# Optimization experiments

Hardware: AMD Instinct MI355X
Metric: run time of the kernel (lower is better)

Reference implementation:

```python
import jax, jax.numpy as jnp
import numpy as np


def setup_inputs() -> dict:
    key = jax.random.key(0)
    k1, k2, k3 = jax.random.split(key, 3)
    N, T, C, H, W, D = 2, 8, 3, 128, 128, 64
    images = jax.random.normal(k1, (N, T, C, H, W), dtype=jnp.float32)
    # well-conditioned pinhole intrinsics: f ~ 100, principal point near center
    K = jnp.array([[100.0, 0.0, W / 2.0], [0.0, 100.0, H / 2.0], [0.0, 0.0, 1.0]], jnp.float32)
    intrinsics = K[None, None] + 0.1 * jax.random.normal(k2, (N, T, 3, 3), dtype=jnp.float32)
    # near-identity extrinsics with small perturbation; last row kept [0,0,0,1]
    E = jnp.eye(4, dtype=jnp.float32)[None, None] + 0.05 * jax.random.normal(k3, (N, T, 4, 4), dtype=jnp.float32)
    extrinsics = E.at[:, :, 3, :].set(jnp.array([0.0, 0.0, 0.0, 1.0], jnp.float32))
    depths = jnp.linspace(1.0, 64.0, D, dtype=jnp.float32)
    return {"images": images, "intrinsics": intrinsics, "extrinsics": extrinsics, "depths": depths}


def _homography_forward(images, intrinsics, extrinsics, depths):
    N, T, C, H, W = images.shape
    D = depths.shape[0]
    dt = images.dtype

    # --- get_homographies ---
    K_ref = intrinsics[:, 0]                      # (N,3,3)
    R_ref = extrinsics[:, 0, :3, :3]              # (N,3,3)
    t_ref = extrinsics[:, 0, :3, 3]               # (N,3)
    n_ref = extrinsics[:, 0, 2, :3]               # (N,3)
    R_view = extrinsics[:, :, :3, :3]             # (N,T,3,3)
    t_view = extrinsics[:, :, :3, 3]              # (N,T,3)

    a = jnp.einsum('nji,nj->ni', R_ref, t_ref)        # R_ref^T t_ref
    b = jnp.einsum('ntji,ntj->nti', R_view, t_view)   # R_view^T t_view
    diff = a[:, None, :] - b                          # (N,T,3)
    t_diff = diff[..., :, None] * n_ref[:, None, None, :]  # outer product -> (N,T,3,3)

    eye = jnp.eye(3, dtype=dt)
    Hmat = eye - t_diff[:, :, None] / depths[None, None, :, None, None]  # (N,T,D,3,3)

    KR = jnp.einsum('ntij,ntjk->ntik', intrinsics, R_view)          # K_view R_view
    world = jnp.einsum('ntij,ntdjk->ntdik', KR, Hmat)               # (N,T,D,3,3)
    ref = jnp.einsum('nij,njk->nik', R_ref, jnp.linalg.inv(K_ref))  # R_ref K_ref^-1
    homog = jnp.einsum('ntdij,njk->ntdik', world, ref)              # (N,T,D,3,3)

    # --- images_to_coords: cartesian_prod(x over W outer, y over H inner, z=1) ---
    x = jnp.arange(W, dtype=dt) + 0.5
    y = jnp.arange(H, dtype=dt) + 0.5
    xs, ys = jnp.meshgrid(x, y, indexing='ij')  # (W,H): x varies slowest
    coords = jnp.stack([xs.ravel(), ys.ravel(), jnp.ones(W * H, dt)], axis=-1)  # (WH,3)

    # --- warp ---
    nc = jnp.einsum('ntdij,pj->ntdpi', homog, coords)  # (N,T,D,WH,3)
    z = nc[..., 2]
    z = jnp.where(z == 0, jnp.asarray(1e-7, dt), z)
    grid = nc[..., :2] / z[..., None]                  # pixel-space coords (faithful: NOT normalized)
    grid = grid.reshape(N * T, D, H, W, 2)

    # --- grid_sample, bilinear, zeros padding, align_corners=False; all D planes at once ---
    gx = ((grid[..., 0] + 1.0) * W - 1.0) * 0.5        # (NT,D,H,W)
    gy = ((grid[..., 1] + 1.0) * H - 1.0) * 0.5
    x0 = jnp.floor(gx); x1 = x0 + 1.0
    y0 = jnp.floor(gy); y1 = y0 + 1.0
    wx1 = gx - x0; wx0 = 1.0 - wx1
    wy1 = gy - y0; wy0 = 1.0 - wy1

    flat = images.reshape(N * T, C, H * W)

    def corner(ix, iy, w):
        valid = (ix >= 0) & (ix <= W - 1) & (iy >= 0) & (iy <= H - 1)
        ii = (jnp.clip(iy, 0, H - 1) * W + jnp.clip(ix, 0, W - 1)).astype(jnp.int32)
        ii = ii.reshape(N * T, -1)                                   # (NT, D*H*W)
        px = jax.vmap(lambda im, idx: im[:, idx])(flat, ii)          # (NT, C, D*H*W)
        return px * (w * valid.astype(dt)).reshape(N * T, 1, -1)

    out = (corner(x0, y0, wx0 * wy0) + corner(x1, y0, wx1 * wy0)
           + corner(x0, y1, wx0 * wy1) + corner(x1, y1, wx1 * wy1))
    return out.reshape(N, T, C, D, H, W)


def reference(images, intrinsics, extrinsics, depths):
    return _homography_forward(images, intrinsics, extrinsics, depths)
```

## Files before the change

### kernel.cpp

```cpp
#include <hip/hip_runtime.h>
#include <hip/hip_bf16.h>

#define Nn 2
#define Tt 8
#define Cc 3
#define Hh 128
#define Ww 128
#define Dd 64
#define NT (Nn * Tt)
#define HW (Hh * Ww)

typedef float f32x4 __attribute__((ext_vector_type(4)));

__global__ __launch_bounds__(256) void homog_fused(
    const float* __restrict__ images,
    const float* __restrict__ intr,
    const float* __restrict__ extr,
    const float* __restrict__ depths,
    float* __restrict__ out)
{
    const int q  = blockIdx.x * 256 + threadIdx.x;
    const int p0 = q << 2;
    const int h  = p0 >> 7;
    const int w  = p0 & 127;
    const int d0 = blockIdx.y << 2;
    const int nt = blockIdx.z;
    const int n  = nt >> 3;

    const float* Kv = intr + nt * 9;
    const float* Kr = intr + (n * Tt) * 9;
    const float* Ev = extr + nt * 16;
    const float* Er = extr + (n * Tt) * 16;

    float Rr[3][3], Rv[3][3], tr[3], tv[3];
    #pragma unroll
    for (int i = 0; i < 3; ++i) {
        #pragma unroll
        for (int j = 0; j < 3; ++j) {
            Rr[i][j] = Er[i * 4 + j];
            Rv[i][j] = Ev[i * 4 + j];
        }
        tr[i] = Er[i * 4 + 3];
        tv[i] = Ev[i * 4 + 3];
    }

    float diff[3];
    #pragma unroll
    for (int i = 0; i < 3; ++i) {
        float a = Rr[0][i] * tr[0] + Rr[1][i] * tr[1] + Rr[2][i] * tr[2];
        float b = Rv[0][i] * tv[0] + Rv[1][i] * tv[1] + Rv[2][i] * tv[2];
        diff[i] = a - b;
    }
    float nr[3] = {Rr[2][0], Rr[2][1], Rr[2][2]};

    float k0 = Kr[0], k1 = Kr[1], k2 = Kr[2];
    float k3 = Kr[3], k4 = Kr[4], k5 = Kr[5];
    float k6 = Kr[6], k7 = Kr[7], k8 = Kr[8];
    float c00 = k4 * k8 - k5 * k7;
    float c01 = k5 * k6 - k3 * k8;
    float c02 = k3 * k7 - k4 * k6;
    float det = k0 * c00 + k1 * c01 + k2 * c02;
    float invd = 1.0f / det;
    float iK[3][3];
    iK[0][0] = c00 * invd;
    iK[0][1] = (k2 * k7 - k1 * k8) * invd;
    iK[0][2] = (k1 * k5 - k2 * k4) * invd;
    iK[1][0] = c01 * invd;
    iK[1][1] = (k0 * k8 - k2 * k6) * invd;
    iK[1][2] = (k2 * k3 - k0 * k5) * invd;
    iK[2][0] = c02 * invd;
    iK[2][1] = (k1 * k6 - k0 * k7) * invd;
    iK[2][2] = (k0 * k4 - k1 * k3) * invd;

    float refM[3][3], KR[3][3];
    #pragma unroll
    for (int i = 0; i < 3; ++i)
        #pragma unroll
        for (int j = 0; j < 3; ++j) {
            refM[i][j] = Rr[i][0] * iK[0][j] + Rr[i][1] * iK[1][j] + Rr[i][2] * iK[2][j];
            KR[i][j]   = Kv[i * 3 + 0] * Rv[0][j] + Kv[i * 3 + 1] * Rv[1][j] + Kv[i * 3 + 2] * Rv[2][j];
        }

    float W0[3][3], u[3], v[3];
    #pragma unroll
    for (int i = 0; i < 3; ++i) {
        #pragma unroll
        for (int j = 0; j < 3; ++j)
            W0[i][j] = KR[i][0] * refM[0][j] + KR[i][1] * refM[1][j] + KR[i][2] * refM[2][j];
        u[i] = KR[i][0] * diff[0] + KR[i][1] * diff[1] + KR[i][2] * diff[2];
        v[i] = refM[0][i] * nr[0] + refM[1][i] * nr[1] + refM[2][i] * nr[2];
    }

    const f32x4 dep4 = *reinterpret_cast<const f32x4*>(&depths[d0]);

    const float xc = (float)h + 0.5f;
    const float yc = (float)w + 0.5f;
    const float* img = images + nt * (Cc * HW);
    const size_t obase_nt = (size_t)(nt * Cc) * Dd * HW + p0;

    #pragma unroll
    for (int dd = 0; dd < 4; ++dd) {
        const float rdep = __builtin_amdgcn_rcpf(dep4[dd]);
        const float u0 = u[0] * rdep, u1 = u[1] * rdep, u2 = u[2] * rdep;
        const float m0 = W0[0][0] - u0 * v[0], m1 = W0[0][1] - u0 * v[1], m2 = W0[0][2] - u0 * v[2];
        const float m3 = W0[1][0] - u1 * v[0], m4 = W0[1][1] - u1 * v[1], m5 = W0[1][2] - u1 * v[2];
        const float m6 = W0[2][0] - u2 * v[0], m7 = W0[2][1] - u2 * v[1], m8 = W0[2][2] - u2 * v[2];

        const float n0 = fmaf(m1, yc, fmaf(m0, xc, m2));
        const float n1 = fmaf(m4, yc, fmaf(m3, xc, m5));
        const float n2 = fmaf(m7, yc, fmaf(m6, xc, m8));

        float r0[4], r1[4], r2[4];
        #pragma unroll
        for (int k = 0; k < 4; ++k) { r0[k] = 0.0f; r1[k] = 0.0f; r2[k] = 0.0f; }

        bool poss[4];
        {
            float a0 = n0, a1 = n1, a2 = n2;
            #pragma unroll
            for (int k = 0; k < 4; ++k) {
                float t = fmaf(1.02f, fabsf(a2), 1e-6f);
                poss[k] = (fabsf(a0) <= t) && (fabsf(a1) <= t);
                a0 += m1; a1 += m4; a2 += m7;
            }
        }

        if (poss[0] || poss[1] || poss[2] || poss[3]) {
            float a0 = n0, a1 = n1, a2 = n2;
            #pragma unroll
            for (int k = 0; k < 4; ++k) {
                if (poss[k]) {
                    float z  = (a2 == 0.0f) ? 1e-7f : a2;
                    float rz = __builtin_amdgcn_rcpf(z);
                    float gx = ((a0 * rz + 1.0f) * (float)Ww - 1.0f) * 0.5f;
                    float gy = ((a1 * rz + 1.0f) * (float)Hh - 1.0f) * 0.5f;

                    float x0f = floorf(gx), y0f = floorf(gy);
                    float x1f = x0f + 1.0f, y1f = y0f + 1.0f;
                    float wx1 = gx - x0f, wx0 = 1.0f - wx1;
                    float wy1 = gy - y0f, wy0 = 1.0f - wy1;

                    float v00 = (x0f >= 0.0f && x0f <= 127.0f && y0f >= 0.0f && y0f <= 127.0f) ? 1.0f : 0.0f;
                    float v10 = (x1f >= 0.0f && x1f <= 127.0f && y0f >= 0.0f && y0f <= 127.0f) ? 1.0f : 0.0f;
                    float v01 = (x0f >= 0.0f && x0f <= 127.0f && y1f >= 0.0f && y1f <= 127.0f) ? 1.0f : 0.0f;
                    float v11 = (x1f >= 0.0f && x1f <= 127.0f && y1f >= 0.0f && y1f <= 127.0f) ? 1.0f : 0.0f;

                    float w00 = (wx0 * wy0) * v00;
                    float w10 = (wx1 * wy0) * v10;
                    float w01 = (wx0 * wy1) * v01;
                    float w11 = (wx1 * wy1) * v11;

                    if (w00 != 0.0f || w10 != 0.0f || w01 != 0.0f || w11 != 0.0f) {
                        int xi0 = (int)fminf(fmaxf(x0f, 0.0f), 127.0f);
                        int xi1 = (int)fminf(fmaxf(x1f, 0.0f), 127.0f);
                        int yi0 = (int)fminf(fmaxf(y0f, 0.0f), 127.0f);
                        int yi1 = (int)fminf(fmaxf(y1f, 0.0f), 127.0f);
                        int i00 = yi0 * Ww + xi0;
                        int i10 = yi0 * Ww + xi1;
                        int i01 = yi1 * Ww + xi0;
                        int i11 = yi1 * Ww + xi1;
                        r0[k] = img[i00] * w00 + img[i10] * w10 + img[i01] * w01 + img[i11] * w11;
                        r1[k] = img[HW + i00] * w00 + img[HW + i10] * w10 + img[HW + i01] * w01 + img[HW + i11] * w11;
                        r2[k] = img[2 * HW + i00] * w00 + img[2 * HW + i10] * w10 + img[2 * HW + i01] * w01 + img[2 * HW + i11] * w11;
                    }
                }
                a0 += m1; a1 += m4; a2 += m7;
            }
        }

        const size_t ob = obase_nt + (size_t)(d0 + dd) * HW;
        f32x4 s0 = {r0[0], r0[1], r0[2], r0[3]};
        f32x4 s1 = {r1[0], r1[1], r1[2], r1[3]};
        f32x4 s2 = {r2[0], r2[1], r2[2], r2[3]};
        __builtin_nontemporal_store(s0, reinterpret_cast<f32x4*>(&out[ob]));
        __builtin_nontemporal_store(s1, reinterpret_cast<f32x4*>(&out[ob + (size_t)Dd * HW]));
        __builtin_nontemporal_store(s2, reinterpret_cast<f32x4*>(&out[ob + (size_t)2 * Dd * HW]));
    }
}

extern "C" void kernel_launch(void* const* d_in, const int* in_sizes, int n_in,
                              void* d_out, int out_size, void* d_ws, size_t ws_size,
                              hipStream_t stream) {
    const float* images = (const float*)d_in[0];
    const float* intr   = (const float*)d_in[1];
    const float* extr   = (const float*)d_in[2];
    const float* depths = (const float*)d_in[3];
    float* out = (float*)d_out;

    homog_fused<<<dim3(HW / 1024, Dd / 4, NT), dim3(256), 0, stream>>>(
        images, intr, extr, depths, out);
}
```

Before: 40.87 us.

## Remap grid to one block per depth plane, looping rows per thread

Each block now handles a whole (nt, depth) plane. Threads loop over 16 row groups, 4 pixels each, instead of each block covering 1024 pixels across 4 depths. The per-block homography setup and the per-depth matrix are computed once per plane and reused across iterations, with row-invariant terms hoisted out. The grid shrinks to 1024 blocks, which cuts redundant setup work but gives fewer blocks for load balancing and latency hiding.

```diff
diff --git a/kernel.cpp b/kernel.cpp
--- a/kernel.cpp
+++ b/kernel.cpp
@@ -12,19 +12,15 @@
 
 typedef float f32x4 __attribute__((ext_vector_type(4)));
 
-__global__ __launch_bounds__(256) void homog_fused(
+__global__ __launch_bounds__(256) void homog_stream(
     const float* __restrict__ images,
     const float* __restrict__ intr,
     const float* __restrict__ extr,
     const float* __restrict__ depths,
     float* __restrict__ out)
 {
-    const int q  = blockIdx.x * 256 + threadIdx.x;
-    const int p0 = q << 2;
-    const int h  = p0 >> 7;
-    const int w  = p0 & 127;
-    const int d0 = blockIdx.y << 2;
-    const int nt = blockIdx.z;
+    const int d  = blockIdx.x;
+    const int nt = blockIdx.y;
     const int n  = nt >> 3;
 
     const float* Kv = intr + nt * 9;
@@ -91,24 +87,28 @@
         v[i] = refM[0][i] * nr[0] + refM[1][i] * nr[1] + refM[2][i] * nr[2];
     }
 
-    const f32x4 dep4 = *reinterpret_cast<const f32x4*>(&depths[d0]);
+    const float rdep = __builtin_amdgcn_rcpf(depths[d]);
+    const float u0 = u[0] * rdep, u1 = u[1] * rdep, u2 = u[2] * rdep;
+    const float m0 = W0[0][0] - u0 * v[0], m1 = W0[0][1] - u0 * v[1], m2 = W0[0][2] - u0 * v[2];
+    const float m3 = W0[1][0] - u1 * v[0], m4 = W0[1][1] - u1 * v[1], m5 = W0[1][2] - u1 * v[2];
+    const float m6 = W0[2][0] - u2 * v[0], m7 = W0[2][1] - u2 * v[1], m8 = W0[2][2] - u2 * v[2];
 
-    const float xc = (float)h + 0.5f;
-    const float yc = (float)w + 0.5f;
+    const int pt = threadIdx.x * 4;
+    const int h0 = pt >> 7;
+    const float yc = (float)(pt & 127) + 0.5f;
+    const float cc0 = fmaf(m1, yc, m2);
+    const float cc1 = fmaf(m4, yc, m5);
+    const float cc2 = fmaf(m7, yc, m8);
+
     const float* img = images + nt * (Cc * HW);
-    const size_t obase_nt = (size_t)(nt * Cc) * Dd * HW + p0;
+    const size_t ob0 = ((size_t)(nt * Cc) * Dd + d) * HW + pt;
 
-    #pragma unroll
-    for (int dd = 0; dd < 4; ++dd) {
-        const float rdep = __builtin_amdgcn_rcpf(dep4[dd]);
-        const float u0 = u[0] * rdep, u1 = u[1] * rdep, u2 = u[2] * rdep;
-        const float m0 = W0[0][0] - u0 * v[0], m1 = W0[0][1] - u0 * v[1], m2 = W0[0][2] - u0 * v[2];
-        const float m3 = W0[1][0] - u1 * v[0], m4 = W0[1][1] - u1 * v[1], m5 = W0[1][2] - u1 * v[2];
-        const float m6 = W0[2][0] - u2 * v[0], m7 = W0[2][1] - u2 * v[1], m8 = W0[2][2] - u2 * v[2];
-
-        const float n0 = fmaf(m1, yc, fmaf(m0, xc, m2));
-        const float n1 = fmaf(m4, yc, fmaf(m3, xc, m5));
-        const float n2 = fmaf(m7, yc, fmaf(m6, xc, m8));
+    #pragma unroll 2
+    for (int it = 0; it < 16; ++it) {
+        const float xc = (float)(h0 + 8 * it) + 0.5f;
+        const float n0 = fmaf(m0, xc, cc0);
+        const float n1 = fmaf(m3, xc, cc1);
+        const float n2 = fmaf(m6, xc, cc2);
 
         float r0[4], r1[4], r2[4];
         #pragma unroll
@@ -168,7 +168,7 @@
             }
         }
 
-        const size_t ob = obase_nt + (size_t)(d0 + dd) * HW;
+        const size_t ob = ob0 + (size_t)it * 1024;
         f32x4 s0 = {r0[0], r0[1], r0[2], r0[3]};
         f32x4 s1 = {r1[0], r1[1], r1[2], r1[3]};
         f32x4 s2 = {r2[0], r2[1], r2[2], r2[3]};
@@ -187,6 +187,6 @@
     const float* depths = (const float*)d_in[3];
     float* out = (float*)d_out;
 
-    homog_fused<<<dim3(HW / 1024, Dd / 4, NT), dim3(256), 0, stream>>>(
+    homog_stream<<<dim3(Dd, NT), dim3(256), 0, stream>>>(
         images, intr, extr, depths, out);
 }
```

Measured after the change: 43.98 us. 7.6% more time.
